# Kernel optimization log

Hardware: AMD Instinct MI355X
Metric: run time of the kernel (lower is better)

## Reference

```python
import jax, jax.numpy as jnp
import numpy as np

N_SAMPLES = 32768
CHANNELS = 128
N_ATOMS = 512
ATOM_SIZE = 512
N_TRANSFERS = 64
TRANSFER_SIZE = 8192
N_EVENTS = 32
N_ROOMS = 8
DILATIONS = (1, 3, 9, 27, 1)
BATCH = 8


def _conv1d(x, w, padding, dil=1):
    # x: [B,C,T], w: [O,I,K]
    return jax.lax.conv_general_dilated(
        x, w, (1,), padding, rhs_dilation=(dil,),
        dimension_numbers=('NCH', 'OIH', 'NCH'))


def _fft_convolve(a, b):
    # linear convolution along last dim, truncated to original length
    n = a.shape[-1]
    af = jnp.fft.rfft(a, n=2 * n)
    bf = jnp.fft.rfft(b, n=2 * n)
    return jnp.fft.irfft(af * bf, n=2 * n)[..., :n]


def _mlp(x, hw, hb, ow, ob):
    # LinearOutputStack: 3 hidden Linear(C,C)+leaky_relu, then Linear(C,out)
    for i in range(hw.shape[0]):
        x = jax.nn.leaky_relu(x @ hw[i] + hb[i], 0.2)
    return x @ ow + ob


def setup_inputs() -> dict:
    key = jax.random.key(0)
    ks = jax.random.split(key, 25)
    s = 0.02
    C = CHANNELS
    return {
        'x': jax.random.normal(ks[0], (BATCH, 1, N_SAMPLES), jnp.float32),
        'bank': jax.random.normal(ks[1], (C, 1, 512), jnp.float32) * s,
        'w_net': jax.random.normal(ks[2], (len(DILATIONS), C, C, 3), jnp.float32) * s,
        'b_net': jnp.zeros((len(DILATIONS), C), jnp.float32),
        'attn_w': jax.random.normal(ks[3], (1, C, 1), jnp.float32) * s,
        'attn_b': jnp.zeros((1,), jnp.float32),
        'atoms_hw': jax.random.normal(ks[4], (3, C, C), jnp.float32) * s,
        'atoms_hb': jnp.zeros((3, C), jnp.float32),
        'atoms_ow': jax.random.normal(ks[5], (C, N_ATOMS), jnp.float32) * s,
        'atoms_ob': jnp.zeros((N_ATOMS,), jnp.float32),
        'trans_hw': jax.random.normal(ks[6], (3, C, C), jnp.float32) * s,
        'trans_hb': jnp.zeros((3, C), jnp.float32),
        'trans_ow': jax.random.normal(ks[7], (C, N_TRANSFERS), jnp.float32) * s,
        'trans_ob': jnp.zeros((N_TRANSFERS,), jnp.float32),
        'amp_hw': jax.random.normal(ks[8], (3, C, C), jnp.float32) * s,
        'amp_hb': jnp.zeros((3, C), jnp.float32),
        'amp_ow': jax.random.normal(ks[9], (C, 1), jnp.float32) * s,
        'amp_ob': jnp.zeros((1,), jnp.float32),
        'atoms_dict': jax.random.uniform(ks[10], (N_ATOMS, ATOM_SIZE), jnp.float32, -1.0, 1.0),
        'transfer_dict': jax.random.normal(ks[11], (N_TRANSFERS, TRANSFER_SIZE), jnp.float32) * 0.01,
        'rooms': jax.random.normal(ks[12], (N_ROOMS, N_SAMPLES), jnp.float32) * 0.01,
        'room_w': jax.random.normal(ks[13], (C, N_ROOMS), jnp.float32) * s,
        'room_b': jnp.zeros((N_ROOMS,), jnp.float32),
        'mix_w': jax.random.normal(ks[14], (C, 1), jnp.float32) * s,
        'mix_b': jnp.zeros((1,), jnp.float32),
    }


def reference(x, bank, w_net, b_net, attn_w, attn_b,
              atoms_hw, atoms_hb, atoms_ow, atoms_ob,
              trans_hw, trans_hb, trans_ow, trans_ob,
              amp_hw, amp_hb, amp_ow, amp_ob,
              atoms_dict, transfer_dict, rooms, room_w, room_b, mix_w, mix_b):
    B = x.shape[0]
    # front-end filter bank, padding=256, truncate to n_samples
    h = _conv1d(x, bank, [(256, 256)])[..., :N_SAMPLES]            # [B,C,T]
    # DilatedStack: residual dilated convs
    for i, d in enumerate(DILATIONS):
        h = h + jax.nn.leaky_relu(
            _conv1d(h, w_net[i], 'SAME', d) + b_net[i][None, :, None], 0.2)
    # ExampleNorm: per-example std normalization
    h = h / (jnp.std(h, axis=(1, 2), keepdims=True) + 1e-8)
    context = jnp.max(h, axis=-1)                                   # [B,C]
    attn = jax.nn.sigmoid(_conv1d(h, attn_w, 'SAME') + attn_b[None, :, None])[:, 0, :]  # [B,T]
    # sparsify_vectors: top-k attention positions, latents scaled by attn
    vals, idx = jax.lax.top_k(attn, N_EVENTS)                        # [B,E]
    lat = jnp.take_along_axis(jnp.swapaxes(h, 1, 2), idx[..., None], axis=1) * vals[..., None]  # [B,E,C]
    atoms = jax.nn.softmax(_mlp(lat, atoms_hw, atoms_hb, atoms_ow, atoms_ob), axis=-1) @ atoms_dict
    transfers = jax.nn.softmax(_mlp(lat, trans_hw, trans_hb, trans_ow, trans_ob), axis=-1) @ transfer_dict
    amps = _mlp(lat, amp_hw, amp_hb, amp_ow, amp_ob) ** 2            # [B,E,1]
    atoms = jnp.pad(atoms, ((0, 0), (0, 0), (0, TRANSFER_SIZE - ATOM_SIZE)))
    ev = (_fft_convolve(atoms, transfers) + atoms) * amps            # [B,E,Ts]
    # overlap-add scatter. NOTE: faithful to the original, which does
    # output[:, :, idx:idx+Ts] += x[i, e] -- every event accumulates into a
    # buffer shared across the whole batch.
    pos = idx.reshape(-1)[:, None] + jnp.arange(TRANSFER_SIZE)[None, :]  # [B*E,Ts]
    buf = jnp.zeros(2 * N_SAMPLES, ev.dtype).at[pos].add(ev.reshape(-1, TRANSFER_SIZE))
    dry = jnp.broadcast_to(buf[:N_SAMPLES][None, :], (B, N_SAMPLES))  # [B,T]
    # ReverbGenerator: context -> room choice + wet/dry mix
    impulse = jax.nn.softmax(context @ room_w + room_b, axis=-1) @ rooms  # [B,T]
    mix = jax.nn.sigmoid(context @ mix_w + mix_b)                     # [B,1]
    wet = _fft_convolve(dry, impulse)
    out = dry * (1.0 - mix) + wet * mix
    return out[:, None, :]
```

## Files before the change

### kernel.cpp

```cpp
#include <hip/hip_runtime.h>
#include <math.h>

#define TSAMP 32768
#define CCH 128
#define NBATCH 8
#define NEV 32
#define NROWS 256
#define NATOMS 512
#define ASIZE 512
#define NTRANS 64
#define TSIZE 8192

#define DRY_SCALE 16777216.0f
#define IMP_SCALE 64.0f
#define WET_DESCALE 9.313225746154785e-10f

#define EPAD(i) ((i) + ((i) >> 5))

typedef _Float16 f16x8 __attribute__((ext_vector_type(8)));
typedef _Float16 f16x4 __attribute__((ext_vector_type(4)));
typedef float f32x4 __attribute__((ext_vector_type(4)));


__global__ __launch_bounds__(256) void k_prep(const float* __restrict__ wn,
                                              const float* __restrict__ bank,
                                              _Float16* __restrict__ whi,
                                              _Float16* __restrict__ wlo,
                                              _Float16* __restrict__ bhi,
                                              _Float16* __restrict__ blo,
                                              double* __restrict__ sums) {
  const int i = blockIdx.x * 256 + threadIdx.x;
  if (i < 16) sums[i] = 0.0;
  if (i < 245760) {
    const int ci = i & 127;
    int r = i >> 7;
    const int o = r & 127;
    r >>= 7;
    const int k = r % 3;
    const int l = r / 3;
    const float w = wn[(((size_t)l*128 + o)*128 + ci)*3 + k];
    const _Float16 hi = (_Float16)w;
    whi[i] = hi;
    wlo[i] = (_Float16)(w - (float)hi);
  } else if (i < 311296) {
    const int j = i - 245760;
    const float w = bank[j];
    const _Float16 hi = (_Float16)w;
    bhi[j] = hi;
    blo[j] = (_Float16)(w - (float)hi);
  }
}

__global__ __launch_bounds__(256) void k_zero(float* __restrict__ wet,
                                              _Float16* __restrict__ drev) {
  int i = blockIdx.x * 256 + threadIdx.x;
  if (i < NBATCH * TSAMP) wet[i] = 0.f;
  if (i < 1088) drev[TSAMP + i] = (_Float16)0.f;
}

__global__ __launch_bounds__(256) void k_front_mfma(
    const float* __restrict__ x, const _Float16* __restrict__ bhi,
    const _Float16* __restrict__ blo, float* __restrict__ h) {
  __shared__ _Float16 shi[8*664];
  __shared__ _Float16 slo[8*664];
  const int t0 = blockIdx.x * 128;
  const int b  = blockIdx.y;
  const float* xb = x + (size_t)b*TSAMP;
  const int tid = threadIdx.x;

  for (int flat = tid; flat < 8*632; flat += 256) {
    const int p = flat / 632;
    const int q = flat - p*632;
    const int g = t0 - 256 + q + p;
    const float v = (g >= 0 && g < TSAMP) ? xb[g] : 0.f;
    const _Float16 hi = (_Float16)v;
    shi[p*664 + q] = hi;
    slo[p*664 + q] = (_Float16)(v - (float)hi);
  }
  __syncthreads();

  const int wv = tid >> 6;
  const int lane = tid & 63;
  const int n = lane & 15;
  const int quad = lane >> 4;
  const int c0 = wv * 32;
  const int ph = n & 7;
  const int nb = n & 8;

  f32x4 acc[2][8];
#pragma unroll
  for (int i = 0; i < 2; ++i)
#pragma unroll
    for (int j = 0; j < 8; ++j) acc[i][j] = (f32x4){0.f,0.f,0.f,0.f};

  for (int kc = 0; kc < 16; ++kc) {
    const int kb = kc*32 + quad*8;
    f16x8 ahi[2], alo[2];
#pragma unroll
    for (int os = 0; os < 2; ++os) {
      const size_t ao = (size_t)(c0 + os*16 + n)*512 + kb;
      ahi[os] = *(const f16x8*)(bhi + ao);
      alo[os] = *(const f16x8*)(blo + ao);
    }
#pragma unroll
    for (int tg = 0; tg < 2; ++tg) {
      f16x8 xh[4], xl[4];
#pragma unroll
      for (int u = 0; u < 4; ++u) {
        const int a = ph*664 + (tg*4 + u)*16 + nb + kb;
        xh[u] = *(const f16x8*)(shi + a);
        xl[u] = *(const f16x8*)(slo + a);
      }
#pragma unroll
      for (int os = 0; os < 2; ++os)
#pragma unroll
        for (int u = 0; u < 4; ++u) {
          f32x4 a4 = acc[os][tg*4 + u];
          a4 = __builtin_amdgcn_mfma_f32_16x16x32_f16(ahi[os], xh[u], a4, 0, 0, 0);
          a4 = __builtin_amdgcn_mfma_f32_16x16x32_f16(alo[os], xh[u], a4, 0, 0, 0);
          a4 = __builtin_amdgcn_mfma_f32_16x16x32_f16(ahi[os], xl[u], a4, 0, 0, 0);
          acc[os][tg*4 + u] = a4;
        }
    }
  }

  float* hb = h + (size_t)b*TSAMP*CCH;
#pragma unroll
  for (int os = 0; os < 2; ++os) {
    const int cb = c0 + os*16 + quad*4;
#pragma unroll
    for (int ts = 0; ts < 8; ++ts) {
      const int t = t0 + ts*16 + n;
      *(f32x4*)(hb + (size_t)t*CCH + cb) = acc[os][ts];
    }
  }
}

__global__ __launch_bounds__(256) void k_dil80(
    const float* __restrict__ hin0, const _Float16* __restrict__ whi,
    const _Float16* __restrict__ wlo, const float* __restrict__ bias,
    float* __restrict__ hout0) {
  const int d = 27;
  extern __shared__ _Float16 sh[];
  const int twin = 80 + 2*d;
  _Float16* shi = sh;
  _Float16* slo = sh + twin*136;
  const int t0 = blockIdx.x * 80;
  const size_t bs = (size_t)blockIdx.y * CCH * TSAMP;
  const float* __restrict__ hin = hin0 + bs;
  float* __restrict__ hout = hout0 + bs;
  const int tid = threadIdx.x;

  for (int flat = tid; flat < twin*32; flat += 256) {
    const int tw = flat >> 5;
    const int c4 = (flat & 31) << 2;
    const int g = t0 - d + tw;
    float4 v = {0.f, 0.f, 0.f, 0.f};
    if (g >= 0 && g < TSAMP) v = *(const float4*)(hin + (size_t)g*CCH + c4);
    f16x4 hv, lv;
    hv[0] = (_Float16)v.x; hv[1] = (_Float16)v.y;
    hv[2] = (_Float16)v.z; hv[3] = (_Float16)v.w;
    lv[0] = (_Float16)(v.x - (float)hv[0]); lv[1] = (_Float16)(v.y - (float)hv[1]);
    lv[2] = (_Float16)(v.z - (float)hv[2]); lv[3] = (_Float16)(v.w - (float)hv[3]);
    *(f16x4*)(shi + tw*136 + c4) = hv;
    *(f16x4*)(slo + tw*136 + c4) = lv;
  }
  __syncthreads();

  const int wv = tid >> 6;
  const int lane = tid & 63;
  const int n = lane & 15;
  const int quad = lane >> 4;
  const int o0 = wv * 32;

  f32x4 acc[2][5];
#pragma unroll
  for (int i = 0; i < 2; ++i)
#pragma unroll
    for (int j = 0; j < 5; ++j) acc[i][j] = (f32x4){0.f,0.f,0.f,0.f};

  for (int k = 0; k < 3; ++k) {
    for (int kc = 0; kc < 4; ++kc) {
      const int cib = kc*32 + quad*8;
      f16x8 ahi[2], alo[2];
#pragma unroll
      for (int os = 0; os < 2; ++os) {
        const size_t wo = ((size_t)k*128 + (o0 + os*16 + n))*128 + cib;
        ahi[os] = *(const f16x8*)(whi + wo);
        alo[os] = *(const f16x8*)(wlo + wo);
      }
      f16x8 bh[5], bl[5];
#pragma unroll
      for (int ts = 0; ts < 5; ++ts) {
        const int a = (ts*16 + n + k*d)*136 + cib;
        bh[ts] = *(const f16x8*)(shi + a);
        bl[ts] = *(const f16x8*)(slo + a);
      }
#pragma unroll
      for (int os = 0; os < 2; ++os)
#pragma unroll
        for (int ts = 0; ts < 5; ++ts) {
          acc[os][ts] = __builtin_amdgcn_mfma_f32_16x16x32_f16(ahi[os], bh[ts], acc[os][ts], 0, 0, 0);
          acc[os][ts] = __builtin_amdgcn_mfma_f32_16x16x32_f16(alo[os], bh[ts], acc[os][ts], 0, 0, 0);
          acc[os][ts] = __builtin_amdgcn_mfma_f32_16x16x32_f16(ahi[os], bl[ts], acc[os][ts], 0, 0, 0);
        }
    }
  }

#pragma unroll
  for (int os = 0; os < 2; ++os) {
    const int ob = o0 + os*16 + quad*4;
    const f32x4 bs4 = *(const f32x4*)(bias + ob);
#pragma unroll
    for (int ts = 0; ts < 5; ++ts) {
      const int t = t0 + ts*16 + n;
      if (t < TSAMP) {
        const int tw = ts*16 + n + d;
        const f16x4 phv = *(const f16x4*)(shi + tw*136 + ob);
        const f16x4 plv = *(const f16x4*)(slo + tw*136 + ob);
        f32x4 res;
#pragma unroll
        for (int r = 0; r < 4; ++r) {
          float v = acc[os][ts][r] + bs4[r];
          v = v > 0.f ? v : 0.2f*v;
          res[r] = (float)phv[r] + (float)plv[r] + v;
        }
        *(f32x4*)(hout + (size_t)t*CCH + ob) = res;
      }
    }
  }
}

__global__ __launch_bounds__(256) void k_dil128(
    const float* __restrict__ hin0, const _Float16* __restrict__ whi,
    const _Float16* __restrict__ wlo, const float* __restrict__ bias,
    float* __restrict__ hout0, const int d) {
  extern __shared__ _Float16 sh[];
  const int twin = 128 + 2*d;
  _Float16* shi = sh;
  _Float16* slo = sh + twin*136;
  const int t0 = blockIdx.x * 128;
  const size_t bs = (size_t)blockIdx.y * CCH * TSAMP;
  const float* __restrict__ hin = hin0 + bs;
  float* __restrict__ hout = hout0 + bs;
  const int tid = threadIdx.x;

  for (int flat = tid; flat < twin*32; flat += 256) {
    const int tw = flat >> 5;
    const int c4 = (flat & 31) << 2;
    const int g = t0 - d + tw;
    float4 v = {0.f, 0.f, 0.f, 0.f};
    if (g >= 0 && g < TSAMP) v = *(const float4*)(hin + (size_t)g*CCH + c4);
    f16x4 hv, lv;
    hv[0] = (_Float16)v.x; hv[1] = (_Float16)v.y;
    hv[2] = (_Float16)v.z; hv[3] = (_Float16)v.w;
    lv[0] = (_Float16)(v.x - (float)hv[0]); lv[1] = (_Float16)(v.y - (float)hv[1]);
    lv[2] = (_Float16)(v.z - (float)hv[2]); lv[3] = (_Float16)(v.w - (float)hv[3]);
    *(f16x4*)(shi + tw*136 + c4) = hv;
    *(f16x4*)(slo + tw*136 + c4) = lv;
  }
  __syncthreads();

  const int wv = tid >> 6;
  const int lane = tid & 63;
  const int n = lane & 15;
  const int quad = lane >> 4;
  const int o0 = wv * 32;

  f32x4 acc[2][8];
#pragma unroll
  for (int i = 0; i < 2; ++i)
#pragma unroll
    for (int j = 0; j < 8; ++j) acc[i][j] = (f32x4){0.f,0.f,0.f,0.f};

  for (int k = 0; k < 3; ++k) {
    for (int kc = 0; kc < 4; ++kc) {
      const int cib = kc*32 + quad*8;
      f16x8 ahi[2], alo[2];
#pragma unroll
      for (int os = 0; os < 2; ++os) {
        const size_t wo = ((size_t)k*128 + (o0 + os*16 + n))*128 + cib;
        ahi[os] = *(const f16x8*)(whi + wo);
        alo[os] = *(const f16x8*)(wlo + wo);
      }
#pragma unroll
      for (int tg = 0; tg < 2; ++tg) {
        f16x8 bh[4], bl[4];
#pragma unroll
        for (int u = 0; u < 4; ++u) {
          const int a = ((tg*4 + u)*16 + n + k*d)*136 + cib;
          bh[u] = *(const f16x8*)(shi + a);
          bl[u] = *(const f16x8*)(slo + a);
        }
#pragma unroll
        for (int os = 0; os < 2; ++os)
#pragma unroll
          for (int u = 0; u < 4; ++u) {
            f32x4 a4 = acc[os][tg*4 + u];
            a4 = __builtin_amdgcn_mfma_f32_16x16x32_f16(ahi[os], bh[u], a4, 0, 0, 0);
            a4 = __builtin_amdgcn_mfma_f32_16x16x32_f16(alo[os], bh[u], a4, 0, 0, 0);
            a4 = __builtin_amdgcn_mfma_f32_16x16x32_f16(ahi[os], bl[u], a4, 0, 0, 0);
            acc[os][tg*4 + u] = a4;
          }
      }
    }
  }

#pragma unroll
  for (int os = 0; os < 2; ++os) {
    const int ob = o0 + os*16 + quad*4;
    const f32x4 bs4 = *(const f32x4*)(bias + ob);
#pragma unroll
    for (int ts = 0; ts < 8; ++ts) {
      const int t = t0 + ts*16 + n;
      const int tw = ts*16 + n + d;
      const f16x4 phv = *(const f16x4*)(shi + tw*136 + ob);
      const f16x4 plv = *(const f16x4*)(slo + tw*136 + ob);
      f32x4 res;
#pragma unroll
      for (int r = 0; r < 4; ++r) {
        float v = acc[os][ts][r] + bs4[r];
        v = v > 0.f ? v : 0.2f*v;
        res[r] = (float)phv[r] + (float)plv[r] + v;
      }
      *(f32x4*)(hout + (size_t)t*CCH + ob) = res;
    }
  }
}

__global__ __launch_bounds__(256) void k_dil_last(
    const float* __restrict__ hin0, const _Float16* __restrict__ whi,
    const _Float16* __restrict__ wlo, const float* __restrict__ bias,
    float* __restrict__ hout0, const int d,
    const float* __restrict__ aw, double* __restrict__ sums,
    float* __restrict__ attnraw, float* __restrict__ pm, const int bb0) {
  extern __shared__ _Float16 sh[];
  const int twin = 128 + 2*d;
  _Float16* shi = sh;
  _Float16* slo = sh + twin*136;
  __shared__ float attl[4*128];
  __shared__ double sred[8];
  const int t0 = blockIdx.x * 128;
  const int b = bb0 + blockIdx.y;
  const size_t bs = (size_t)blockIdx.y * CCH * TSAMP;
  const float* __restrict__ hin = hin0 + bs;
  float* __restrict__ hout = hout0 + bs;
  const int tid = threadIdx.x;

  for (int flat = tid; flat < twin*32; flat += 256) {
    const int tw = flat >> 5;
    const int c4 = (flat & 31) << 2;
    const int g = t0 - d + tw;
    float4 v = {0.f, 0.f, 0.f, 0.f};
    if (g >= 0 && g < TSAMP) v = *(const float4*)(hin + (size_t)g*CCH + c4);
    f16x4 hv, lv;
    hv[0] = (_Float16)v.x; hv[1] = (_Float16)v.y;
    hv[2] = (_Float16)v.z; hv[3] = (_Float16)v.w;
    lv[0] = (_Float16)(v.x - (float)hv[0]); lv[1] = (_Float16)(v.y - (float)hv[1]);
    lv[2] = (_Float16)(v.z - (float)hv[2]); lv[3] = (_Float16)(v.w - (float)hv[3]);
    *(f16x4*)(shi + tw*136 + c4) = hv;
    *(f16x4*)(slo + tw*136 + c4) = lv;
  }
  __syncthreads();

  const int wv = tid >> 6;
  const int lane = tid & 63;
  const int n = lane & 15;
  const int quad = lane >> 4;
  const int o0 = wv * 32;

  f32x4 acc[2][8];
#pragma unroll
  for (int i = 0; i < 2; ++i)
#pragma unroll
    for (int j = 0; j < 8; ++j) acc[i][j] = (f32x4){0.f,0.f,0.f,0.f};

  for (int k = 0; k < 3; ++k) {
    for (int kc = 0; kc < 4; ++kc) {
      const int cib = kc*32 + quad*8;
      f16x8 ahi[2], alo[2];
#pragma unroll
      for (int os = 0; os < 2; ++os) {
        const size_t wo = ((size_t)k*128 + (o0 + os*16 + n))*128 + cib;
        ahi[os] = *(const f16x8*)(whi + wo);
        alo[os] = *(const f16x8*)(wlo + wo);
      }
#pragma unroll
      for (int tg = 0; tg < 2; ++tg) {
        f16x8 bh[4], bl[4];
#pragma unroll
        for (int u = 0; u < 4; ++u) {
          const int a = ((tg*4 + u)*16 + n + k*d)*136 + cib;
          bh[u] = *(const f16x8*)(shi + a);
          bl[u] = *(const f16x8*)(slo + a);
        }
#pragma unroll
        for (int os = 0; os < 2; ++os)
#pragma unroll
          for (int u = 0; u < 4; ++u) {
            f32x4 a4 = acc[os][tg*4 + u];
            a4 = __builtin_amdgcn_mfma_f32_16x16x32_f16(ahi[os], bh[u], a4, 0, 0, 0);
            a4 = __builtin_amdgcn_mfma_f32_16x16x32_f16(alo[os], bh[u], a4, 0, 0, 0);
            a4 = __builtin_amdgcn_mfma_f32_16x16x32_f16(ahi[os], bl[u], a4, 0, 0, 0);
            acc[os][tg*4 + u] = a4;
          }
      }
    }
  }

  const f32x4 awq0 = *(const f32x4*)(aw + o0 + quad*4);
  const f32x4 awq1 = *(const f32x4*)(aw + o0 + 16 + quad*4);
  double s = 0.0, s2 = 0.0;
  float pa[8] = {0.f,0.f,0.f,0.f,0.f,0.f,0.f,0.f};
  f32x4 cm[2];
  cm[0] = (f32x4){-3.4e38f, -3.4e38f, -3.4e38f, -3.4e38f};
  cm[1] = cm[0];

#pragma unroll
  for (int os = 0; os < 2; ++os) {
    const int ob = o0 + os*16 + quad*4;
    const f32x4 bs4 = *(const f32x4*)(bias + ob);
    const f32x4 awv = os ? awq1 : awq0;
#pragma unroll
    for (int ts = 0; ts < 8; ++ts) {
      const int t = t0 + ts*16 + n;
      const int tw = ts*16 + n + d;
      const f16x4 phv = *(const f16x4*)(shi + tw*136 + ob);
      const f16x4 plv = *(const f16x4*)(slo + tw*136 + ob);
      f32x4 res;
      float dotp = 0.f;
#pragma unroll
      for (int r = 0; r < 4; ++r) {
        float v = acc[os][ts][r] + bs4[r];
        v = v > 0.f ? v : 0.2f*v;
        const float hv = (float)phv[r] + (float)plv[r] + v;
        res[r] = hv;
        s += (double)hv; s2 += (double)hv*(double)hv;
        dotp += hv * awv[r];
        cm[os][r] = fmaxf(cm[os][r], hv);
      }
      pa[ts] += dotp;
      *(f32x4*)(hout + (size_t)t*CCH + ob) = res;
    }
  }

#pragma unroll
  for (int ts = 0; ts < 8; ++ts) {
    pa[ts] += __shfl_xor(pa[ts], 16);
    pa[ts] += __shfl_xor(pa[ts], 32);
  }
  if (quad == 0) {
#pragma unroll
    for (int ts = 0; ts < 8; ++ts) attl[wv*128 + ts*16 + n] = pa[ts];
  }
#pragma unroll
  for (int mk = 1; mk <= 8; mk <<= 1)
#pragma unroll
    for (int os = 0; os < 2; ++os)
#pragma unroll
      for (int r = 0; r < 4; ++r)
        cm[os][r] = fmaxf(cm[os][r], __shfl_xor(cm[os][r], mk));
  if (n == 0) {
#pragma unroll
    for (int os = 0; os < 2; ++os)
      *(f32x4*)(pm + ((size_t)b*256 + blockIdx.x)*128 + o0 + os*16 + quad*4) = cm[os];
  }
  for (int sft = 32; sft; sft >>= 1) { s += __shfl_down(s, sft); s2 += __shfl_down(s2, sft); }
  if (lane == 0) { sred[wv*2] = s; sred[wv*2+1] = s2; }
  __syncthreads();
  if (tid < 128)
    attnraw[(size_t)b*TSAMP + t0 + tid] =
        attl[tid] + attl[128 + tid] + attl[256 + tid] + attl[384 + tid];
  if (tid == 0) {
    atomicAdd(&sums[b*2],   sred[0] + sred[2] + sred[4] + sred[6]);
    atomicAdd(&sums[b*2+1], sred[1] + sred[3] + sred[5] + sred[7]);
  }
}

__global__ __launch_bounds__(128) void k_finish(
    const double* __restrict__ sums, const float* __restrict__ pm,
    const float* __restrict__ room_w, const float* __restrict__ room_b,
    const float* __restrict__ mix_w, const float* __restrict__ mix_b,
    float* __restrict__ scal, float* __restrict__ roomp, float* __restrict__ mix) {
  const int b = blockIdx.x;
  const int tid = threadIdx.x;
  __shared__ float bs;
  __shared__ float ctx[128];
  if (tid == 0) {
    const double nn = (double)CCH * (double)TSAMP;
    const double mean = sums[b*2] / nn;
    double var = sums[b*2+1] / nn - mean*mean;
    if (var < 0.0) var = 0.0;
    const float sc = (float)(1.0 / (sqrt(var) + 1e-8));
    bs = sc;
    scal[b] = sc;
  }
  __syncthreads();
  float m = -3.4e38f;
  for (int s = 0; s < 256; ++s) m = fmaxf(m, pm[((size_t)b*256 + s)*128 + tid]);
  ctx[tid] = m * bs;
  __syncthreads();
  if (tid < 8) {
    const int r = tid;
    float acc = room_b[r];
    for (int c = 0; c < CCH; ++c) acc += ctx[c] * room_w[c*8 + r];
    float mm = acc;
    for (int s = 1; s < 8; s <<= 1) mm = fmaxf(mm, __shfl_xor(mm, s, 8));
    const float e = expf(acc - mm);
    float ss = e;
    for (int s = 1; s < 8; s <<= 1) ss += __shfl_xor(ss, s, 8);
    roomp[b*8 + r] = e / ss;
  } else if (tid == 8) {
    float a = mix_b[0];
    for (int c = 0; c < CCH; ++c) a += ctx[c] * mix_w[c];
    mix[b] = 1.f/(1.f+expf(-a));
  }
}

__global__ __launch_bounds__(256) void k_topk1(const float* __restrict__ raw,
                                               const float* __restrict__ scal,
                                               const float* __restrict__ ab,
                                               float* __restrict__ cv,
                                               int* __restrict__ cidx) {
  const int ch = blockIdx.x, b = blockIdx.y;
  const float sc = scal[b], bb_ = ab[0];
  const float* a = raw + (size_t)b*TSAMP + ch*2048;
  __shared__ float v[2048];
  __shared__ float rv[4]; __shared__ int ri[4];
  const int tid = threadIdx.x;
  for (int i = tid; i < 2048; i += 256)
    v[i] = 1.f/(1.f+expf(-(a[i]*sc + bb_)));
  __syncthreads();
  for (int e = 0; e < NEV; ++e) {
    float bv = -1e30f; int bi = 0;
    for (int i = tid; i < 2048; i += 256) {
      const float x = v[i];
      if (x > bv) { bv = x; bi = i; }
    }
    for (int s = 32; s; s >>= 1) {
      const float ov = __shfl_down(bv, s); const int oi = __shfl_down(bi, s);
      if (ov > bv || (ov == bv && oi < bi)) { bv = ov; bi = oi; }
    }
    if ((tid & 63) == 0) { rv[tid >> 6] = bv; ri[tid >> 6] = bi; }
    __syncthreads();
    if (tid == 0) {
      int bb = 0;
      for (int w2 = 1; w2 < 4; ++w2)
        if (rv[w2] > rv[bb] || (rv[w2] == rv[bb] && ri[w2] < ri[bb])) bb = w2;
      cv[(b*16 + ch)*NEV + e] = rv[bb];
      cidx[(b*16 + ch)*NEV + e] = ch*2048 + ri[bb];
      v[ri[bb]] = -1e30f;
    }
    __syncthreads();
  }
}

__global__ __launch_bounds__(512) void k_topk2(const float* __restrict__ cv,
                                               const int* __restrict__ ci_,
                                               float* __restrict__ vals,
                                               int* __restrict__ idxs) {
  const int b = blockIdx.x;
  const int tid = threadIdx.x;
  float my = cv[b*512 + tid];
  int   mi = ci_[b*512 + tid];
  __shared__ float rv[8]; __shared__ int ri[8];
  __shared__ float bvs; __shared__ int bis;
  for (int e = 0; e < NEV; ++e) {
    float bv = my; int bi = mi;
    for (int s = 32; s; s >>= 1) {
      const float ov = __shfl_down(bv, s); const int oi = __shfl_down(bi, s);
      if (ov > bv || (ov == bv && oi < bi)) { bv = ov; bi = oi; }
    }
    if ((tid & 63) == 0) { rv[tid >> 6] = bv; ri[tid >> 6] = bi; }
    __syncthreads();
    if (tid == 0) {
      int bb = 0;
      for (int w2 = 1; w2 < 8; ++w2)
        if (rv[w2] > rv[bb] || (rv[w2] == rv[bb] && ri[w2] < ri[bb])) bb = w2;
      vals[b*NEV + e] = rv[bb]; idxs[b*NEV + e] = ri[bb];
      bvs = rv[bb]; bis = ri[bb];
    }
    __syncthreads();
    if (mi == bis && my == bvs) my = -1e30f;
    __syncthreads();
  }
}

__device__ __forceinline__ float blk_max128(float v, float* red) {
  const int tid = threadIdx.x;
  red[tid] = v; __syncthreads();
  for (int s = 64; s > 0; s >>= 1) {
    if (tid < s) red[tid] = fmaxf(red[tid], red[tid + s]);
    __syncthreads();
  }
  const float r = red[0]; __syncthreads();
  return r;
}
__device__ __forceinline__ float blk_sum128(float v, float* red) {
  const int tid = threadIdx.x;
  red[tid] = v; __syncthreads();
  for (int s = 64; s > 0; s >>= 1) {
    if (tid < s) red[tid] += red[tid + s];
    __syncthreads();
  }
  const float r = red[0]; __syncthreads();
  return r;
}
__device__ __forceinline__ float mlp_hidden3(float latv, const float* __restrict__ hw,
                                             const float* __restrict__ hb, float* xa) {
  const int tid = threadIdx.x;
  float cur = latv;
  for (int i = 0; i < 3; ++i) {
    xa[tid] = cur; __syncthreads();
    const float* W = hw + (size_t)i*CCH*CCH;
    float acc = hb[i*CCH + tid];
    for (int c = 0; c < CCH; ++c) acc += xa[c] * W[c*CCH + tid];
    cur = acc > 0.f ? acc : 0.2f*acc;
    __syncthreads();
  }
  return cur;
}

__global__ __launch_bounds__(128) void k_mlp(
    const float* __restrict__ h, const float* __restrict__ scal,
    const float* __restrict__ vals, const int* __restrict__ idxs,
    const float* __restrict__ a_hw, const float* __restrict__ a_hb,
    const float* __restrict__ a_ow, const float* __restrict__ a_ob,
    const float* __restrict__ t_hw, const float* __restrict__ t_hb,
    const float* __restrict__ t_ow, const float* __restrict__ t_ob,
    const float* __restrict__ m_hw, const float* __restrict__ m_hb,
    const float* __restrict__ m_ow, const float* __restrict__ m_ob,
    float* __restrict__ p_atoms, float* __restrict__ p_trans, float* __restrict__ amps) {
  const int row = blockIdx.x;
  const int b = row >> 5;
  const int tid = threadIdx.x;
  __shared__ float xa[CCH];
  __shared__ float red[CCH];
  const int t = idxs[row];
  const float latv = h[((size_t)b*TSAMP + t)*CCH + tid] * scal[b] * vals[row];

  {
    const float cur = mlp_hidden3(latv, a_hw, a_hb, xa);
    xa[tid] = cur; __syncthreads();
    float l0 = a_ob[tid], l1 = a_ob[tid+128], l2 = a_ob[tid+256], l3 = a_ob[tid+384];
    for (int c = 0; c < CCH; ++c) {
      const float xv = xa[c];
      const float* W = a_ow + (size_t)c*NATOMS + tid;
      l0 += xv*W[0]; l1 += xv*W[128]; l2 += xv*W[256]; l3 += xv*W[384];
    }
    const float mx = blk_max128(fmaxf(fmaxf(l0,l1), fmaxf(l2,l3)), red);
    const float e0 = expf(l0-mx), e1 = expf(l1-mx), e2 = expf(l2-mx), e3 = expf(l3-mx);
    const float inv = 1.f / blk_sum128(e0+e1+e2+e3, red);
    float* pa = p_atoms + (size_t)row*NATOMS;
    pa[tid] = e0*inv; pa[tid+128] = e1*inv; pa[tid+256] = e2*inv; pa[tid+384] = e3*inv;
  }
  {
    const float cur = mlp_hidden3(latv, t_hw, t_hb, xa);
    xa[tid] = cur; __syncthreads();
    float lg = -3.4e38f;
    if (tid < NTRANS) {
      float acc = t_ob[tid];
      for (int c = 0; c < CCH; ++c) acc += xa[c]*t_ow[c*NTRANS + tid];
      lg = acc;
    }
    const float mt = blk_max128(lg, red);
    const float et = (tid < NTRANS) ? expf(lg - mt) : 0.f;
    const float st = blk_sum128(et, red);
    if (tid < NTRANS) p_trans[(size_t)row*NTRANS + tid] = et/st;
  }
  {
    const float cur = mlp_hidden3(latv, m_hw, m_hb, xa);
    const float s = blk_sum128(cur * m_ow[tid], red);
    if (tid == 0) { const float v = s + m_ob[0]; amps[row] = v*v; }
  }
}

__global__ __launch_bounds__(256) void k_atoms_mm(const float* __restrict__ p_atoms,
                                                  const float* __restrict__ dict,
                                                  float* __restrict__ av) {
  const int row = blockIdx.x;
  __shared__ float p[NATOMS];
  for (int i = threadIdx.x; i < NATOMS; i += 256) p[i] = p_atoms[(size_t)row*NATOMS + i];
  __syncthreads();
  const int s0 = threadIdx.x*2;
  float a0=0, a1=0;
  for (int a = 0; a < NATOMS; ++a) {
    const float pa = p[a];
    const float2 dv = *(const float2*)(dict + (size_t)a*ASIZE + s0);
    a0 += pa*dv.x; a1 += pa*dv.y;
  }
  av[(size_t)row*ASIZE + s0] = a0; av[(size_t)row*ASIZE + s0 + 1] = a1;
}

__global__ __launch_bounds__(256) void k_trans_mm(const float* __restrict__ p_trans,
                                                   const float* __restrict__ td,
                                                   float* __restrict__ trans) {
  const int row = blockIdx.y;
  const int t = blockIdx.x*2048 + threadIdx.x*8;
  __shared__ float p[NTRANS];
  if (threadIdx.x < NTRANS) p[threadIdx.x] = p_trans[(size_t)row*NTRANS + threadIdx.x];
  __syncthreads();
  float a0=0,a1=0,a2=0,a3=0,a4=0,a5=0,a6=0,a7=0;
  for (int j = 0; j < NTRANS; ++j) {
    const float pj = p[j];
    const float4 v0 = *(const float4*)(td + (size_t)j*TSIZE + t);
    const float4 v1 = *(const float4*)(td + (size_t)j*TSIZE + t + 4);
    a0 += pj*v0.x; a1 += pj*v0.y; a2 += pj*v0.z; a3 += pj*v0.w;
    a4 += pj*v1.x; a5 += pj*v1.y; a6 += pj*v1.z; a7 += pj*v1.w;
  }
  float* o = trans + (size_t)row*TSIZE + t;
  o[0]=a0; o[1]=a1; o[2]=a2; o[3]=a3; o[4]=a4; o[5]=a5; o[6]=a6; o[7]=a7;
}

__global__ __launch_bounds__(256) void k_ev(const float* __restrict__ trans,
                                            const float* __restrict__ av,
                                            const float* __restrict__ amps,
                                            float* __restrict__ ev) {
  const int row = blockIdx.y;
  const int t0 = blockIdx.x * 1024;
  __shared__ float al[512];
  __shared__ float tw[1584];
  for (int i = threadIdx.x; i < 512; i += 256) al[i] = av[(size_t)row*ASIZE + i];
  for (int i = threadIdx.x; i < 1536; i += 256) {
    const int g = t0 - 512 + i;
    tw[EPAD(i)] = (g >= 0) ? trans[(size_t)row*TSIZE + g] : 0.f;
  }
  __syncthreads();
  const int base = threadIdx.x*4 + 512;
  float a0=0,a1=0,a2=0,a3=0;
  float w0=tw[EPAD(base)], w1=tw[EPAD(base+1)], w2=tw[EPAD(base+2)], w3=tw[EPAD(base+3)];
#pragma unroll 8
  for (int k = 0; k < 512; ++k) {
    const float ak = al[k];
    a0 += ak*w0; a1 += ak*w1; a2 += ak*w2; a3 += ak*w3;
    w3 = w2; w2 = w1; w1 = w0;
    const int p = base - k - 1;
    w0 = tw[EPAD(p)];
  }
  const int n = t0 + threadIdx.x*4;
  const float amp = amps[row];
  float* e = ev + (size_t)row*TSIZE + n;
  e[0] = (a0 + (n+0 < 512 ? al[n+0] : 0.f)) * amp;
  e[1] = (a1 + (n+1 < 512 ? al[n+1] : 0.f)) * amp;
  e[2] = (a2 + (n+2 < 512 ? al[n+2] : 0.f)) * amp;
  e[3] = (a3 + (n+3 < 512 ? al[n+3] : 0.f)) * amp;
}

__global__ __launch_bounds__(256) void k_dry(const float* __restrict__ ev,
                                             const int* __restrict__ idxs,
                                             float* __restrict__ dry,
                                             _Float16* __restrict__ drev) {
  __shared__ int sidx[NROWS];
  if (threadIdx.x < NROWS) sidx[threadIdx.x] = idxs[threadIdx.x];
  __syncthreads();
  const int p = blockIdx.x*256 + threadIdx.x;
  float a = 0.f;
  for (int r = 0; r < NROWS; ++r) {
    const int off = p - sidx[r];
    if ((unsigned)off < TSIZE) a += ev[(size_t)r*TSIZE + off];
  }
  dry[p] = a;
  drev[TSAMP - 1 - p] = (_Float16)(a * DRY_SCALE);
}

__global__ __launch_bounds__(256) void k_impulse(const float* __restrict__ roomp,
                                                 const float* __restrict__ rooms,
                                                 _Float16* __restrict__ ihi) {
  const int b = blockIdx.y;
  const int t = blockIdx.x*1024 + threadIdx.x*4;
  float a0=0,a1=0,a2=0,a3=0;
  for (int r = 0; r < 8; ++r) {
    const float pr = roomp[b*8 + r];
    const float4 v = *(const float4*)(rooms + (size_t)r*TSAMP + t);
    a0 += pr*v.x; a1 += pr*v.y; a2 += pr*v.z; a3 += pr*v.w;
  }
  _Float16* oh = ihi + (size_t)b*TSAMP + t;
  oh[0] = (_Float16)(a0*IMP_SCALE); oh[1] = (_Float16)(a1*IMP_SCALE);
  oh[2] = (_Float16)(a2*IMP_SCALE); oh[3] = (_Float16)(a3*IMP_SCALE);
}

__global__ __launch_bounds__(256) void k_wet_mfma(
    const _Float16* __restrict__ drev, const _Float16* __restrict__ ihi,
    float* __restrict__ wet) {
  const int t0 = blockIdx.x * 512;
  const int k0 = blockIdx.y * 4096;
  if (k0 > t0 + 511) return;
  __shared__ _Float16 rhi[8*1048];
  const int tid = threadIdx.x;
  const int wv = tid >> 6;
  const int lane = tid & 63;
  const int n16 = lane & 15;
  const int quad = lane >> 4;
  const int m = n16;

  f32x4 acc[8];
#pragma unroll
  for (int j = 0; j < 8; ++j) acc[j] = (f32x4){0.f,0.f,0.f,0.f};

  const int kend = (k0 + 4096 < t0 + 512) ? k0 + 4096 : t0 + 512;
  const int ph = 7 - (n16 & 7);
  for (int kc0 = k0; kc0 < kend; kc0 += 512) {
    const int RB = TSAMP - 1 - (t0 + 511 - kc0);
    for (int flat = tid; flat < 8*1016; flat += 256) {
      const int p = flat / 1016;
      const int q = flat - p*1016;
      rhi[p*1048 + q] = drev[RB + p + q];
    }
    __syncthreads();

#pragma unroll 4
    for (int kc = 0; kc < 16; ++kc) {
      const int kb = kc*32;
      const int jg = kc0 + kb + quad*8;
      f16x8 ah;
      if (m < NBATCH) ah = *(const f16x8*)(ihi + (size_t)m*TSAMP + jg);
      else ah = (f16x8){0,0,0,0,0,0,0,0};
#pragma unroll
      for (int ts = 0; ts < 8; ++ts) {
        const int nn = wv*128 + ts*16 + n16;
        const int a = ph*1048 + kb + quad*8 + 504 - (nn & ~7);
        const f16x8 bh = *(const f16x8*)(rhi + a);
        acc[ts] = __builtin_amdgcn_mfma_f32_16x16x32_f16(ah, bh, acc[ts], 0, 0, 0);
      }
    }
    __syncthreads();
  }

#pragma unroll
  for (int ts = 0; ts < 8; ++ts) {
    const int t = t0 + wv*128 + ts*16 + n16;
#pragma unroll
    for (int r = 0; r < 4; ++r) {
      const int b = quad*4 + r;
      if (b < NBATCH)
        atomicAdd(wet + (size_t)b*TSAMP + t, acc[ts][r] * WET_DESCALE);
    }
  }
}

__global__ __launch_bounds__(256) void k_out(const float* __restrict__ dry,
                                             const float* __restrict__ wet,
                                             const float* __restrict__ mix,
                                             float* __restrict__ out) {
  const int b = blockIdx.y;
  const int t = blockIdx.x*1024 + threadIdx.x*4;
  const float m = mix[b];
  const float4 d = *(const float4*)(dry + t);
  const float4 w = *(const float4*)(wet + (size_t)b*TSAMP + t);
  float* o = out + (size_t)b*TSAMP + t;
  o[0] = d.x*(1.f-m) + w.x*m;
  o[1] = d.y*(1.f-m) + w.y*m;
  o[2] = d.z*(1.f-m) + w.z*m;
  o[3] = d.w*(1.f-m) + w.w*m;
}

extern "C" void kernel_launch(void* const* d_in, const int* in_sizes, int n_in,
                              void* d_out, int out_size, void* d_ws, size_t ws_size,
                              hipStream_t stream) {
  (void)in_sizes; (void)n_in; (void)out_size;
  const float* x      = (const float*)d_in[0];
  const float* bank   = (const float*)d_in[1];
  const float* w_net  = (const float*)d_in[2];
  const float* b_net  = (const float*)d_in[3];
  const float* attn_w = (const float*)d_in[4];
  const float* attn_b = (const float*)d_in[5];
  const float* a_hw = (const float*)d_in[6];
  const float* a_hb = (const float*)d_in[7];
  const float* a_ow = (const float*)d_in[8];
  const float* a_ob = (const float*)d_in[9];
  const float* t_hw = (const float*)d_in[10];
  const float* t_hb = (const float*)d_in[11];
  const float* t_ow = (const float*)d_in[12];
  const float* t_ob = (const float*)d_in[13];
  const float* m_hw = (const float*)d_in[14];
  const float* m_hb = (const float*)d_in[15];
  const float* m_ow = (const float*)d_in[16];
  const float* m_ob = (const float*)d_in[17];
  const float* atoms_dict    = (const float*)d_in[18];
  const float* transfer_dict = (const float*)d_in[19];
  const float* rooms  = (const float*)d_in[20];
  const float* room_w = (const float*)d_in[21];
  const float* room_b = (const float*)d_in[22];
  const float* mix_w  = (const float*)d_in[23];
  const float* mix_b  = (const float*)d_in[24];
  float* out = (float*)d_out;

  float* ws = (float*)d_ws;
  const size_t need4 = (size_t)67944480 * 4;
  const int NB = (ws_size >= need4) ? 4 : 2;
  const size_t S = (size_t)CCH * TSAMP;
  float* H  = ws;
  float* t1 = ws + (size_t)33554432;
  float* t2 = ws + 33554432 + NB*S;
  const size_t w_off = 33554432 + 2*(size_t)NB*S;
  _Float16* whi = (_Float16*)(ws + w_off);
  _Float16* wlo = whi + 245760;
  _Float16* bhi = wlo + 245760;
  _Float16* blo = bhi + 65536;
  double* sums  = (double*)(ws + w_off + 311296);
  float* attnraw = ws + w_off + 311296 + 32;
  float* pm      = attnraw + (size_t)NBATCH*TSAMP;

  size_t off = 33554432;
  float* scal  = ws + off; off += 8;
  float* vals  = ws + off; off += NROWS;
  int*   idxs  = (int*)(ws + off); off += NROWS;
  float* p_atoms = ws + off; off += (size_t)NROWS*NATOMS;
  float* p_trans = ws + off; off += (size_t)NROWS*NTRANS;
  float* amps  = ws + off; off += NROWS;
  float* av    = ws + off; off += (size_t)NROWS*ASIZE;
  float* trans = ws + off; off += (size_t)NROWS*TSIZE;
  float* ev    = ws + off; off += (size_t)NROWS*TSIZE;
  float* dry   = ws + off; off += TSAMP;
  float* roomp = ws + off; off += 64;
  float* mix   = ws + off; off += 8;
  float* wet   = ws + off; off += (size_t)NBATCH*TSAMP;
  float* cand_v = ws + off; off += 4096;
  int*   cand_i = (int*)(ws + off); off += 4096;
  _Float16* imphi = (_Float16*)(ws + off); off += (size_t)NBATCH*TSAMP/2;
  _Float16* drev  = (_Float16*)(ws + off); off += (TSAMP + 1088)/2 + 4;

  k_prep<<<1216, 256, 0, stream>>>(w_net, bank, whi, wlo, bhi, blo, sums);
  k_front_mfma<<<dim3(256, 8), 256, 0, stream>>>(x, bhi, blo, H);

  const int dil[5] = {1, 3, 9, 27, 1};
  const int npairs = 8 / NB;
  for (int p = 0; p < npairs; ++p) {
    float* Hp = H + (size_t)(NB*p) * S;
    float* io[6] = {Hp, t1, t2, t1, t2, Hp};
    for (int i = 0; i < 3; ++i) {
      const int d = dil[i];
      const size_t smem = (size_t)(128 + 2*d) * 544;
      k_dil128<<<dim3(256, NB), 256, smem, stream>>>(
          io[i], whi + (size_t)i*49152, wlo + (size_t)i*49152, b_net + i*CCH,
          io[i+1], d);
    }
    {
      const size_t smem = (size_t)134 * 544;
      k_dil80<<<dim3(410, NB), 256, smem, stream>>>(
          io[3], whi + (size_t)3*49152, wlo + (size_t)3*49152, b_net + 3*CCH,
          io[4]);
    }
    {
      const int d = dil[4];
      const size_t smem = (size_t)(128 + 2*d) * 544;
      k_dil_last<<<dim3(256, NB), 256, smem, stream>>>(
          io[4], whi + (size_t)4*49152, wlo + (size_t)4*49152, b_net + 4*CCH,
          io[5], d, attn_w, sums, attnraw, pm, NB*p);
    }
  }

  k_zero<<<1024, 256, 0, stream>>>(wet, drev);
  k_finish<<<8, 128, 0, stream>>>(sums, pm, room_w, room_b, mix_w, mix_b,
                                  scal, roomp, mix);
  k_topk1<<<dim3(16, 8), 256, 0, stream>>>(attnraw, scal, attn_b, cand_v, cand_i);
  k_topk2<<<8, 512, 0, stream>>>(cand_v, cand_i, vals, idxs);
  k_mlp<<<256, 128, 0, stream>>>(H, scal, vals, idxs,
                                 a_hw, a_hb, a_ow, a_ob,
                                 t_hw, t_hb, t_ow, t_ob,
                                 m_hw, m_hb, m_ow, m_ob,
                                 p_atoms, p_trans, amps);
  k_atoms_mm<<<256, 256, 0, stream>>>(p_atoms, atoms_dict, av);
  k_trans_mm<<<dim3(4, 256), 256, 0, stream>>>(p_trans, transfer_dict, trans);
  k_ev<<<dim3(8, 256), 256, 0, stream>>>(trans, av, amps, ev);
  k_dry<<<128, 256, 0, stream>>>(ev, idxs, dry, drev);
  k_impulse<<<dim3(32, 8), 256, 0, stream>>>(roomp, rooms, imphi);
  k_wet_mfma<<<dim3(64, 8), 256, 0, stream>>>(drev, imphi, wet);
  k_out<<<dim3(32, 8), 256, 0, stream>>>(dry, wet, mix, out);
}
```

Before: 1.205 ms.

## Fix batch grouping at two, add 96-wide dilation-1 kernel, widen k_dry grid

Removes the workspace-dependent choice of processing four batch items per pass and always processes two, with fixed workspace offsets. The first dilated conv layer now uses a new 96-timestep tile kernel with 342 blocks per batch, which gives more blocks and better CU coverage when only two batches run per launch. k_dry now runs 256 blocks of 128 threads instead of 128 of 256 so more CUs take part. The trade-off is more kernel launches per layer, since four passes replace the two used when four batches fit.

```diff
diff --git a/kernel.cpp b/kernel.cpp
--- a/kernel.cpp
+++ b/kernel.cpp
@@ -328,6 +328,102 @@
   }
 }
 
+__global__ __launch_bounds__(256) void k_dil96(
+    const float* __restrict__ hin0, const _Float16* __restrict__ whi,
+    const _Float16* __restrict__ wlo, const float* __restrict__ bias,
+    float* __restrict__ hout0, const int d) {
+  extern __shared__ _Float16 sh[];
+  const int twin = 96 + 2*d;
+  _Float16* shi = sh;
+  _Float16* slo = sh + twin*136;
+  const int t0 = blockIdx.x * 96;
+  const size_t bs = (size_t)blockIdx.y * CCH * TSAMP;
+  const float* __restrict__ hin = hin0 + bs;
+  float* __restrict__ hout = hout0 + bs;
+  const int tid = threadIdx.x;
+
+  for (int flat = tid; flat < twin*32; flat += 256) {
+    const int tw = flat >> 5;
+    const int c4 = (flat & 31) << 2;
+    const int g = t0 - d + tw;
+    float4 v = {0.f, 0.f, 0.f, 0.f};
+    if (g >= 0 && g < TSAMP) v = *(const float4*)(hin + (size_t)g*CCH + c4);
+    f16x4 hv, lv;
+    hv[0] = (_Float16)v.x; hv[1] = (_Float16)v.y;
+    hv[2] = (_Float16)v.z; hv[3] = (_Float16)v.w;
+    lv[0] = (_Float16)(v.x - (float)hv[0]); lv[1] = (_Float16)(v.y - (float)hv[1]);
+    lv[2] = (_Float16)(v.z - (float)hv[2]); lv[3] = (_Float16)(v.w - (float)hv[3]);
+    *(f16x4*)(shi + tw*136 + c4) = hv;
+    *(f16x4*)(slo + tw*136 + c4) = lv;
+  }
+  __syncthreads();
+
+  const int wv = tid >> 6;
+  const int lane = tid & 63;
+  const int n = lane & 15;
+  const int quad = lane >> 4;
+  const int o0 = wv * 32;
+
+  f32x4 acc[2][6];
+#pragma unroll
+  for (int i = 0; i < 2; ++i)
+#pragma unroll
+    for (int j = 0; j < 6; ++j) acc[i][j] = (f32x4){0.f,0.f,0.f,0.f};
+
+  for (int k = 0; k < 3; ++k) {
+    for (int kc = 0; kc < 4; ++kc) {
+      const int cib = kc*32 + quad*8;
+      f16x8 ahi[2], alo[2];
+#pragma unroll
+      for (int os = 0; os < 2; ++os) {
+        const size_t wo = ((size_t)k*128 + (o0 + os*16 + n))*128 + cib;
+        ahi[os] = *(const f16x8*)(whi + wo);
+        alo[os] = *(const f16x8*)(wlo + wo);
+      }
+      f16x8 bh[6], bl[6];
+#pragma unroll
+      for (int u = 0; u < 6; ++u) {
+        const int a = (u*16 + n + k*d)*136 + cib;
+        bh[u] = *(const f16x8*)(shi + a);
+        bl[u] = *(const f16x8*)(slo + a);
+      }
+#pragma unroll
+      for (int os = 0; os < 2; ++os)
+#pragma unroll
+        for (int u = 0; u < 6; ++u) {
+          f32x4 a4 = acc[os][u];
+          a4 = __builtin_amdgcn_mfma_f32_16x16x32_f16(ahi[os], bh[u], a4, 0, 0, 0);
+          a4 = __builtin_amdgcn_mfma_f32_16x16x32_f16(alo[os], bh[u], a4, 0, 0, 0);
+          a4 = __builtin_amdgcn_mfma_f32_16x16x32_f16(ahi[os], bl[u], a4, 0, 0, 0);
+          acc[os][u] = a4;
+        }
+    }
+  }
+
+#pragma unroll
+  for (int os = 0; os < 2; ++os) {
+    const int ob = o0 + os*16 + quad*4;
+    const f32x4 bs4 = *(const f32x4*)(bias + ob);
+#pragma unroll
+    for (int ts = 0; ts < 6; ++ts) {
+      const int t = t0 + ts*16 + n;
+      if (t < TSAMP) {
+        const int tw = ts*16 + n + d;
+        const f16x4 phv = *(const f16x4*)(shi + tw*136 + ob);
+        const f16x4 plv = *(const f16x4*)(slo + tw*136 + ob);
+        f32x4 res;
+#pragma unroll
+        for (int r = 0; r < 4; ++r) {
+          float v = acc[os][ts][r] + bs4[r];
+          v = v > 0.f ? v : 0.2f*v;
+          res[r] = (float)phv[r] + (float)plv[r] + v;
+        }
+        *(f32x4*)(hout + (size_t)t*CCH + ob) = res;
+      }
+    }
+  }
+}
+
 __global__ __launch_bounds__(256) void k_dil_last(
     const float* __restrict__ hin0, const _Float16* __restrict__ whi,
     const _Float16* __restrict__ wlo, const float* __restrict__ bias,
@@ -746,14 +842,17 @@
   e[3] = (a3 + (n+3 < 512 ? al[n+3] : 0.f)) * amp;
 }
 
-__global__ __launch_bounds__(256) void k_dry(const float* __restrict__ ev,
+__global__ __launch_bounds__(128) void k_dry(const float* __restrict__ ev,
                                              const int* __restrict__ idxs,
                                              float* __restrict__ dry,
                                              _Float16* __restrict__ drev) {
   __shared__ int sidx[NROWS];
-  if (threadIdx.x < NROWS) sidx[threadIdx.x] = idxs[threadIdx.x];
-  __syncthreads();
-  const int p = blockIdx.x*256 + threadIdx.x;
+  if (threadIdx.x < 128) {
+    sidx[threadIdx.x] = idxs[threadIdx.x];
+    sidx[threadIdx.x + 128] = idxs[threadIdx.x + 128];
+  }
+  __syncthreads();
+  const int p = blockIdx.x*128 + threadIdx.x;
   float a = 0.f;
   for (int r = 0; r < NROWS; ++r) {
     const int off = p - sidx[r];
@@ -857,7 +956,7 @@
 extern "C" void kernel_launch(void* const* d_in, const int* in_sizes, int n_in,
                               void* d_out, int out_size, void* d_ws, size_t ws_size,
                               hipStream_t stream) {
-  (void)in_sizes; (void)n_in; (void)out_size;
+  (void)in_sizes; (void)n_in; (void)out_size; (void)ws_size;
   const float* x      = (const float*)d_in[0];
   const float* bank   = (const float*)d_in[1];
   const float* w_net  = (const float*)d_in[2];
@@ -886,19 +985,16 @@
   float* out = (float*)d_out;
 
   float* ws = (float*)d_ws;
-  const size_t need4 = (size_t)67944480 * 4;
-  const int NB = (ws_size >= need4) ? 4 : 2;
   const size_t S = (size_t)CCH * TSAMP;
   float* H  = ws;
   float* t1 = ws + (size_t)33554432;
-  float* t2 = ws + 33554432 + NB*S;
-  const size_t w_off = 33554432 + 2*(size_t)NB*S;
-  _Float16* whi = (_Float16*)(ws + w_off);
+  float* t2 = ws + (size_t)41943040;
+  _Float16* whi = (_Float16*)(ws + (size_t)50331648);
   _Float16* wlo = whi + 245760;
   _Float16* bhi = wlo + 245760;
   _Float16* blo = bhi + 65536;
-  double* sums  = (double*)(ws + w_off + 311296);
-  float* attnraw = ws + w_off + 311296 + 32;
+  double* sums   = (double*)(ws + (size_t)50642944);
+  float* attnraw = ws + (size_t)50642976;
   float* pm      = attnraw + (size_t)NBATCH*TSAMP;
 
   size_t off = 33554432;
@@ -924,29 +1020,33 @@
   k_front_mfma<<<dim3(256, 8), 256, 0, stream>>>(x, bhi, blo, H);
 
   const int dil[5] = {1, 3, 9, 27, 1};
-  const int npairs = 8 / NB;
-  for (int p = 0; p < npairs; ++p) {
-    float* Hp = H + (size_t)(NB*p) * S;
+  for (int p = 0; p < 4; ++p) {
+    float* Hp = H + (size_t)(2*p) * S;
     float* io[6] = {Hp, t1, t2, t1, t2, Hp};
-    for (int i = 0; i < 3; ++i) {
+    {
+      const size_t smem = (size_t)98 * 544;
+      k_dil96<<<dim3(342, 2), 256, smem, stream>>>(
+          io[0], whi, wlo, b_net, io[1], 1);
+    }
+    for (int i = 1; i < 3; ++i) {
       const int d = dil[i];
       const size_t smem = (size_t)(128 + 2*d) * 544;
-      k_dil128<<<dim3(256, NB), 256, smem, stream>>>(
+      k_dil128<<<dim3(256, 2), 256, smem, stream>>>(
           io[i], whi + (size_t)i*49152, wlo + (size_t)i*49152, b_net + i*CCH,
           io[i+1], d);
     }
     {
       const size_t smem = (size_t)134 * 544;
-      k_dil80<<<dim3(410, NB), 256, smem, stream>>>(
+      k_dil80<<<dim3(410, 2), 256, smem, stream>>>(
           io[3], whi + (size_t)3*49152, wlo + (size_t)3*49152, b_net + 3*CCH,
           io[4]);
     }
     {
       const int d = dil[4];
       const size_t smem = (size_t)(128 + 2*d) * 544;
-      k_dil_last<<<dim3(256, NB), 256, smem, stream>>>(
+      k_dil_last<<<dim3(256, 2), 256, smem, stream>>>(
           io[4], whi + (size_t)4*49152, wlo + (size_t)4*49152, b_net + 4*CCH,
-          io[5], d, attn_w, sums, attnraw, pm, NB*p);
+          io[5], d, attn_w, sums, attnraw, pm, 2*p);
     }
   }
 
@@ -963,7 +1063,7 @@
   k_atoms_mm<<<256, 256, 0, stream>>>(p_atoms, atoms_dict, av);
   k_trans_mm<<<dim3(4, 256), 256, 0, stream>>>(p_trans, transfer_dict, trans);
   k_ev<<<dim3(8, 256), 256, 0, stream>>>(trans, av, amps, ev);
-  k_dry<<<128, 256, 0, stream>>>(ev, idxs, dry, drev);
+  k_dry<<<256, 128, 0, stream>>>(ev, idxs, dry, drev);
   k_impulse<<<dim3(32, 8), 256, 0, stream>>>(roomp, rooms, imphi);
   k_wet_mfma<<<dim3(64, 8), 256, 0, stream>>>(drev, imphi, wet);
   k_out<<<dim3(32, 8), 256, 0, stream>>>(dry, wet, mix, out);
```

New measurement: 1.263 ms. 4.9% more time.
